# Performance work log

Hardware: AMD Instinct MI355X
Metric: run time of the kernel (lower is better)

The kernel has to match this reference:

```python
import jax, jax.numpy as jnp
import numpy as np

HEADS = 8
DIM_HEAD = 64
SCALE = DIM_HEAD ** -0.5


def setup_inputs() -> dict:
    key = jax.random.key(0)
    ks = jax.random.split(key, 6)
    B, S, D = 4, 2048, 512
    return {
        "hidden_states": jax.random.normal(ks[0], (B, S, D), jnp.float32),
        "Wq": jax.random.normal(ks[1], (D, D), jnp.float32) * (D ** -0.5),
        "Wk": jax.random.normal(ks[2], (D, D), jnp.float32) * (D ** -0.5),
        "Wv": jax.random.normal(ks[3], (D, D), jnp.float32) * (D ** -0.5),
        "Wo": jax.random.normal(ks[4], (D, D), jnp.float32) * (D ** -0.5),
        "bo": jnp.zeros((D,), jnp.float32),
    }


def reference(hidden_states, Wq, Wk, Wv, Wo, bo):
    B, S, D = hidden_states.shape
    H, Dh = HEADS, DIM_HEAD
    # Linear projections (torch Linear: x @ W.T; weights here stored as [D, D] used directly)
    q = hidden_states @ Wq  # [B,S,D]
    k = hidden_states @ Wk
    v = hidden_states @ Wv
    # head_to_batch_dim: [B,S,D] -> [B,H,S,Dh]
    q = q.reshape(B, S, H, Dh).transpose(0, 2, 1, 3)
    k = k.reshape(B, S, H, Dh).transpose(0, 2, 1, 3)
    v = v.reshape(B, S, H, Dh).transpose(0, 2, 1, 3)
    # scaled dot-product attention, scores materialized as in baddbmm path
    scores = jnp.einsum("bhqd,bhkd->bhqk", q, k) * SCALE  # [B,H,S,S]
    probs = jax.nn.softmax(scores, axis=-1)
    out = jnp.einsum("bhqk,bhkd->bhqd", probs, v)  # [B,H,S,Dh]
    # batch_to_head_dim: [B,H,S,Dh] -> [B,S,D]
    out = out.transpose(0, 2, 1, 3).reshape(B, S, D)
    # output projection (Dropout with p=0 is identity)
    return out @ Wo + bo
```

## Files before the change

kernel.cpp:

```cpp
#include <hip/hip_runtime.h>
#include <cstdint>
#include <cstddef>


typedef __bf16 bf16;
typedef __bf16 bf16x4_t __attribute__((ext_vector_type(4)));
typedef __bf16 bf16x8_t __attribute__((ext_vector_type(8)));
typedef float  floatx4  __attribute__((ext_vector_type(4)));
typedef short  shortx4  __attribute__((ext_vector_type(4)));
typedef uint32_t u32x4  __attribute__((ext_vector_type(4)));

#define NB   4
#define SEQ  2048
#define DM   512
#define NH   8
#define DH   64
#define MTOT (NB * SEQ)


__device__ __forceinline__ void gload16(const void* g, void* l) {
    __builtin_amdgcn_global_load_lds((const __attribute__((address_space(1))) unsigned int*)g,
                                     (__attribute__((address_space(3))) unsigned int*)l,
                                     16, 0, 0);
}

__device__ __forceinline__ shortx4 pack4(floatx4 v) {
    union { bf16x4_t h; shortx4 s; } u;
    u.h = (bf16x4_t){ (bf16)v[0], (bf16)v[1], (bf16)v[2], (bf16)v[3] };
    return u.s;
}

__global__ __launch_bounds__(256) void cvt_x(const float* __restrict__ x, bf16* __restrict__ xb) {
    int i = (blockIdx.x * 256 + threadIdx.x) * 4;
    float4 v = *(const float4*)(x + i);
    bf16x4_t o = { (bf16)v.x, (bf16)v.y, (bf16)v.z, (bf16)v.w };
    *(bf16x4_t*)(xb + i) = o;
}

__global__ __launch_bounds__(256) void prep_w(const float* __restrict__ Wq, const float* __restrict__ Wk,
                                              const float* __restrict__ Wv, const float* __restrict__ Wo,
                                              bf16* __restrict__ Wqkvt, bf16* __restrict__ Wot) {
    __shared__ float T[64][65];
    const int tid = threadIdx.x;
    const int m = blockIdx.z;
    const int k0 = blockIdx.x * 64, n0 = blockIdx.y * 64;
    const float* W = (m == 0) ? Wq : (m == 1) ? Wk : (m == 2) ? Wv : Wo;
    const float scale = (m == 0) ? 0.18033688011112042f : 1.0f;
#pragma unroll
    for (int p = 0; p < 4; p++) {
        int row = p * 16 + (tid >> 4), col = (tid & 15) * 4;
        float4 v = *(const float4*)(W + (size_t)(k0 + row) * DM + n0 + col);
        T[row][col + 0] = v.x * scale; T[row][col + 1] = v.y * scale;
        T[row][col + 2] = v.z * scale; T[row][col + 3] = v.w * scale;
    }
    __syncthreads();
#pragma unroll
    for (int p = 0; p < 4; p++) {
        int nr = p * 16 + (tid >> 4), kc = (tid & 15) * 4;
        bf16x4_t o = { (bf16)T[kc][nr], (bf16)T[kc + 1][nr], (bf16)T[kc + 2][nr], (bf16)T[kc + 3][nr] };
        bf16* dst = (m < 3) ? (Wqkvt + ((size_t)(m * DM + n0 + nr)) * DM + k0 + kc)
                            : (Wot + (size_t)(n0 + nr) * DM + k0 + kc);
        *(bf16x4_t*)dst = o;
    }
}

__global__ __launch_bounds__(256) void gemm_qkv(
        const bf16* __restrict__ A, const bf16* __restrict__ Bt,
        bf16* __restrict__ Qh, bf16* __restrict__ Kh, bf16* __restrict__ Vt) {
    __shared__ __attribute__((aligned(16))) bf16 Sm[2][128 * 64];
    bf16* As = Sm[0]; bf16* Bs = Sm[1];
    const int tid = threadIdx.x;
    const int wave = tid >> 6, lane = tid & 63;
    const int l15 = lane & 15, quad = lane >> 4, h7 = l15 & 7;
    const int m0 = blockIdx.x * 128, n0 = blockIdx.y * 128;
    const int mw = (wave >> 1) * 64, nw = (wave & 1) * 64;
    const int srow = lane >> 3, sc = (lane & 7) ^ srow;

    floatx4 zero = {0.f, 0.f, 0.f, 0.f};
    floatx4 acc[4][4];
#pragma unroll
    for (int i = 0; i < 4; i++)
#pragma unroll
        for (int j = 0; j < 4; j++) acc[i][j] = zero;

    for (int k0 = 0; k0 < DM; k0 += 64) {
#pragma unroll
        for (int t = 0; t < 4; t++) {
            int row = wave * 32 + t * 8 + srow;
            gload16(A  + (size_t)(m0 + row) * DM + k0 + sc * 8, As + (wave * 32 + t * 8) * 64);
            gload16(Bt + (size_t)(n0 + row) * DM + k0 + sc * 8, Bs + (wave * 32 + t * 8) * 64);
        }
        __syncthreads();
#pragma unroll
        for (int ks = 0; ks < 2; ks++) {
            bf16x8_t af[4], bfr[4];
#pragma unroll
            for (int i = 0; i < 4; i++)
                af[i] = *(const bf16x8_t*)(As + (mw + i * 16 + l15) * 64 + (((ks * 4 + quad) ^ h7) * 8));
#pragma unroll
            for (int j = 0; j < 4; j++)
                bfr[j] = *(const bf16x8_t*)(Bs + (nw + j * 16 + l15) * 64 + (((ks * 4 + quad) ^ h7) * 8));
#pragma unroll
            for (int i = 0; i < 4; i++)
#pragma unroll
                for (int j = 0; j < 4; j++)
                    acc[i][j] = __builtin_amdgcn_mfma_f32_16x16x32_bf16(af[i], bfr[j], acc[i][j], 0, 0, 0);
        }
        __syncthreads();
    }

    bf16* E = (bf16*)Sm;
    const int sect = n0 >> 9;
    const int bq = m0 >> 11;
    if (sect < 3 && (n0 >> 9) != 2) {}
    if (sect != 2) {
        bf16* dstbase = (sect == 0) ? Qh : Kh;
#pragma unroll
        for (int p = 0; p < 2; p++) {
            if ((wave >> 1) == p) {
#pragma unroll
                for (int i = 0; i < 4; i++)
#pragma unroll
                    for (int j = 0; j < 4; j++)
#pragma unroll
                        for (int r = 0; r < 4; r++)
                            E[(i * 16 + quad * 4 + r) * 136 + nw + j * 16 + l15] = (bf16)acc[i][j][r];
            }
            __syncthreads();
#pragma unroll
            for (int pp = 0; pp < 4; pp++) {
                int idx = pp * 256 + tid;
                int rowl = idx >> 4, chunk = idx & 15;
                u32x4 v = *(const u32x4*)(E + rowl * 136 + chunk * 8);
                int mm = m0 + p * 64 + rowl;
                int s = mm & (SEQ - 1);
                int n = n0 + chunk * 8;
                int h = (n >> 6) & 7, d = n & 63;
                *(u32x4*)(dstbase + (((size_t)(bq * NH + h)) * SEQ + s) * DH + d) = v;
            }
            __syncthreads();
        }
    } else {
#pragma unroll
        for (int p = 0; p < 2; p++) {
            if ((wave & 1) == p) {
#pragma unroll
                for (int i = 0; i < 4; i++)
#pragma unroll
                    for (int j = 0; j < 4; j++)
                        *(shortx4*)(E + (j * 16 + l15) * 136 + mw + i * 16 + quad * 4) = pack4(acc[i][j]);
            }
            __syncthreads();
#pragma unroll
            for (int pp = 0; pp < 4; pp++) {
                int idx = pp * 256 + tid;
                int rowl = idx >> 4, chunk = idx & 15;
                u32x4 v = *(const u32x4*)(E + rowl * 136 + chunk * 8);
                int n = n0 + p * 64 + rowl;
                int h = (n >> 6) & 7, d = n & 63;
                int s = (m0 & (SEQ - 1)) + chunk * 8;
                *(u32x4*)(Vt + (((size_t)(bq * NH + h)) * DH + d) * SEQ + s) = v;
            }
            __syncthreads();
        }
    }
}

__global__ __launch_bounds__(256) void gemm_out(
        const bf16* __restrict__ A, const bf16* __restrict__ Bt,
        const float* __restrict__ bo, float* __restrict__ out) {
    __shared__ __attribute__((aligned(16))) bf16 As[64 * 64];
    __shared__ __attribute__((aligned(16))) bf16 Bs[128 * 64];
    const int tid = threadIdx.x;
    const int wave = tid >> 6, lane = tid & 63;
    const int l15 = lane & 15, quad = lane >> 4, h7 = l15 & 7;
    const int m0 = blockIdx.x * 64, n0 = blockIdx.y * 128;
    const int nw = wave * 32;
    const int srow = lane >> 3, sc = (lane & 7) ^ srow;

    floatx4 zero = {0.f, 0.f, 0.f, 0.f};
    floatx4 acc[4][2];
#pragma unroll
    for (int i = 0; i < 4; i++)
#pragma unroll
        for (int j = 0; j < 2; j++) acc[i][j] = zero;

    for (int k0 = 0; k0 < DM; k0 += 64) {
#pragma unroll
        for (int t = 0; t < 2; t++) {
            int row = wave * 16 + t * 8 + srow;
            gload16(A + (size_t)(m0 + row) * DM + k0 + sc * 8, As + (wave * 16 + t * 8) * 64);
        }
#pragma unroll
        for (int t = 0; t < 4; t++) {
            int row = wave * 32 + t * 8 + srow;
            gload16(Bt + (size_t)(n0 + row) * DM + k0 + sc * 8, Bs + (wave * 32 + t * 8) * 64);
        }
        __syncthreads();
#pragma unroll
        for (int ks = 0; ks < 2; ks++) {
            bf16x8_t af[4], bfr[2];
#pragma unroll
            for (int i = 0; i < 4; i++)
                af[i] = *(const bf16x8_t*)(As + (i * 16 + l15) * 64 + (((ks * 4 + quad) ^ h7) * 8));
#pragma unroll
            for (int j = 0; j < 2; j++)
                bfr[j] = *(const bf16x8_t*)(Bs + (nw + j * 16 + l15) * 64 + (((ks * 4 + quad) ^ h7) * 8));
#pragma unroll
            for (int i = 0; i < 4; i++)
#pragma unroll
                for (int j = 0; j < 2; j++)
                    acc[i][j] = __builtin_amdgcn_mfma_f32_16x16x32_bf16(af[i], bfr[j], acc[i][j], 0, 0, 0);
        }
        __syncthreads();
    }
#pragma unroll
    for (int i = 0; i < 4; i++)
#pragma unroll
        for (int j = 0; j < 2; j++)
#pragma unroll
            for (int r = 0; r < 4; r++) {
                int m = m0 + i * 16 + quad * 4 + r;
                int n = n0 + nw + j * 16 + l15;
                out[(size_t)m * DM + n] = acc[i][j][r] + bo[n];
            }
}

__global__ __launch_bounds__(256, 2) void flash_attn(
        const bf16* __restrict__ Q, const bf16* __restrict__ Kh,
        const bf16* __restrict__ Vt, bf16* __restrict__ Ob) {
    __shared__ __attribute__((aligned(16))) bf16 SMEM[4 * 8192];
    const int tid = threadIdx.x;
    const int wave = tid >> 6, lane = tid & 63;
    const int l15 = lane & 15, quad = lane >> 4, h7 = l15 & 7;
    const int qh = wave >> 1, kvh = wave & 1;
    const int qt = blockIdx.x & 15, bh = blockIdx.x >> 4;
    const int q0 = qt * 128;
    const bf16* Kb = Kh + (size_t)bh * SEQ * DH;
    const bf16* Vb = Vt + (size_t)bh * DH * SEQ;

    bf16x8_t aq[4][2];
#pragma unroll
    for (int sub = 0; sub < 4; sub++) {
        const bf16* qr = Q + ((size_t)bh * SEQ + q0 + qh * 64 + sub * 16 + l15) * DH;
        aq[sub][0] = *(const bf16x8_t*)(qr + quad * 8);
        aq[sub][1] = *(const bf16x8_t*)(qr + 32 + quad * 8);
    }

    const int srow = lane >> 3, sc = (lane & 7) ^ srow;
    auto stage = [&](int buf, int kv0) {
#pragma unroll
        for (int t = 0; t < 2; t++) {
            int rb = wave * 16 + t * 8;
            gload16(Kb + (size_t)(kv0 + rb + srow) * DH + sc * 8, SMEM + buf * 8192 + rb * 64);
            gload16(Vb + (size_t)(rb + srow) * SEQ + kv0 + sc * 8, SMEM + buf * 8192 + 4096 + rb * 64);
        }
    };

    floatx4 zero = {0.f, 0.f, 0.f, 0.f};
    floatx4 oacc[4][4];
    float l_run[4] = {0.f, 0.f, 0.f, 0.f};
#pragma unroll
    for (int sub = 0; sub < 4; sub++)
#pragma unroll
        for (int d = 0; d < 4; d++) oacc[sub][d] = zero;

    stage(0, 0);
    stage(1, 64);
    for (int seg = 0; seg < 16; seg++) {
        __syncthreads();
        if (seg < 15) {
            stage((2 * seg + 2) & 3, (2 * seg + 2) * 64);
            stage((2 * seg + 3) & 3, (2 * seg + 3) * 64);
        }
#pragma unroll
        for (int half = 0; half < 2; half++) {
            const bf16* Ks = SMEM + ((2 * seg + half) & 3) * 8192;
            const bf16* Vs = Ks + 4096;
            floatx4 st[4][2];
#pragma unroll
            for (int nsl = 0; nsl < 2; nsl++) {
                int row = (kvh * 2 + nsl) * 16 + l15;
                const bf16* kr = Ks + row * 64;
                bf16x8_t k0 = *(const bf16x8_t*)(kr + ((quad ^ h7) * 8));
                bf16x8_t k1 = *(const bf16x8_t*)(kr + (((4 + quad) ^ h7) * 8));
#pragma unroll
                for (int sub = 0; sub < 4; sub++) {
                    floatx4 a = zero;
                    a = __builtin_amdgcn_mfma_f32_16x16x32_bf16(k0, aq[sub][0], a, 0, 0, 0);
                    a = __builtin_amdgcn_mfma_f32_16x16x32_bf16(k1, aq[sub][1], a, 0, 0, 0);
                    st[sub][nsl] = a;
                }
            }
#pragma unroll
            for (int sub = 0; sub < 4; sub++) {
                float s = 0.f;
#pragma unroll
                for (int nsl = 0; nsl < 2; nsl++)
#pragma unroll
                    for (int r = 0; r < 4; r++) {
                        float p = __builtin_amdgcn_exp2f(st[sub][nsl][r]);
                        st[sub][nsl][r] = p;
                        s += p;
                    }
                l_run[sub] += s;
            }
#pragma unroll
            for (int cl = 0; cl < 2; cl++) {
                int c = kvh * 2 + cl;
                shortx4 ap[4];
#pragma unroll
                for (int sub = 0; sub < 4; sub++) ap[sub] = pack4(st[sub][cl]);
                int cc = 2 * c + (quad >> 1);
#pragma unroll
                for (int d = 0; d < 4; d++) {
                    const bf16* vr = Vs + (d * 16 + l15) * 64;
                    shortx4 bv = *(const shortx4*)(vr + ((cc ^ h7) * 8) + (quad & 1) * 4);
#pragma unroll
                    for (int sub = 0; sub < 4; sub++)
                        oacc[sub][d] = __builtin_amdgcn_mfma_f32_16x16x16bf16_1k(ap[sub], bv, oacc[sub][d], 0, 0, 0);
                }
            }
        }
    }

    float lf[4];
#pragma unroll
    for (int sub = 0; sub < 4; sub++) {
        float l = l_run[sub];
        l += __shfl_xor(l, 16, 64);
        l += __shfl_xor(l, 32, 64);
        lf[sub] = l;
    }
    __syncthreads();
    float* blob = (float*)SMEM + qh * (68 * 64);
    if (kvh == 1) {
#pragma unroll
        for (int sub = 0; sub < 4; sub++)
#pragma unroll
            for (int d = 0; d < 4; d++)
#pragma unroll
                for (int r = 0; r < 4; r++)
                    blob[((sub * 4 + d) * 4 + r) * 64 + lane] = oacc[sub][d][r];
#pragma unroll
        for (int sub = 0; sub < 4; sub++)
            blob[(64 + sub) * 64 + lane] = lf[sub];
    }
    __syncthreads();
    if (kvh == 0) {
#pragma unroll
        for (int sub = 0; sub < 4; sub++)
#pragma unroll
            for (int d = 0; d < 4; d++)
#pragma unroll
                for (int r = 0; r < 4; r++)
                    oacc[sub][d][r] += blob[((sub * 4 + d) * 4 + r) * 64 + lane];
#pragma unroll
        for (int sub = 0; sub < 4; sub++)
            lf[sub] += blob[(64 + sub) * 64 + lane];

        const int b = bh >> 3, h = bh & 7;
#pragma unroll
        for (int sub = 0; sub < 4; sub++) {
            float linv[4];
#pragma unroll
            for (int r = 0; r < 4; r++) linv[r] = 1.0f / __shfl(lf[sub], quad * 4 + r, 64);
#pragma unroll
            for (int d = 0; d < 4; d++)
#pragma unroll
                for (int r = 0; r < 4; r++) {
                    int s = q0 + qh * 64 + sub * 16 + quad * 4 + r;
                    Ob[((size_t)b * SEQ + s) * DM + h * DH + d * 16 + l15] = (bf16)(oacc[sub][d][r] * linv[r]);
                }
        }
    }
}

extern "C" void kernel_launch(void* const* d_in, const int* in_sizes, int n_in,
                              void* d_out, int out_size, void* d_ws, size_t ws_size,
                              hipStream_t stream) {
    const float* X  = (const float*)d_in[0];
    const float* Wq = (const float*)d_in[1];
    const float* Wk = (const float*)d_in[2];
    const float* Wv = (const float*)d_in[3];
    const float* Wo = (const float*)d_in[4];
    const float* bo = (const float*)d_in[5];
    float* out = (float*)d_out;

    char* ws = (char*)d_ws;
    bf16* Xb    = (bf16*)(ws + 0);
    bf16* Wqkvt = (bf16*)(ws + 8388608);
    bf16* Wot   = (bf16*)(ws + 9961472);
    bf16* Qh    = (bf16*)(ws + 10485760);
    bf16* Kh    = (bf16*)(ws + 18874368);
    bf16* Vt    = (bf16*)(ws + 27262976);
    bf16* Ob    = (bf16*)(ws + 35651584);

    cvt_x<<<MTOT * DM / 1024, 256, 0, stream>>>(X, Xb);
    prep_w<<<dim3(8, 8, 4), 256, 0, stream>>>(Wq, Wk, Wv, Wo, Wqkvt, Wot);
    gemm_qkv<<<dim3(MTOT / 128, 1536 / 128), 256, 0, stream>>>(Xb, Wqkvt, Qh, Kh, Vt);
    flash_attn<<<NB * NH * (SEQ / 128), 256, 0, stream>>>(Qh, Kh, Vt, Ob);
    gemm_out<<<dim3(MTOT / 64, DM / 128), 256, 0, stream>>>(Ob, Wot, bo, out);
}
```

Baseline: 160.7 us.

## Halve attention LDS to raise occupancy, merge prep kernels into one launch

Flash attention now double-buffers single 64-row KV tiles instead of quad-buffering pairs, which halves shared memory. Its launch bound rises from 2 to 4 blocks per SM. The final cross-wave reduction is split into two phases so it fits in the smaller LDS buffer. The X-conversion and weight-prep kernels are merged into one launch to cut launch overhead. The risks are register spills under the tighter launch bound and less prefetch depth to hide memory latency.

```diff
diff --git a/kernel.cpp b/kernel.cpp
--- a/kernel.cpp
+++ b/kernel.cpp
@@ -30,20 +30,23 @@
     return u.s;
 }
 
-__global__ __launch_bounds__(256) void cvt_x(const float* __restrict__ x, bf16* __restrict__ xb) {
-    int i = (blockIdx.x * 256 + threadIdx.x) * 4;
-    float4 v = *(const float4*)(x + i);
-    bf16x4_t o = { (bf16)v.x, (bf16)v.y, (bf16)v.z, (bf16)v.w };
-    *(bf16x4_t*)(xb + i) = o;
-}
-
-__global__ __launch_bounds__(256) void prep_w(const float* __restrict__ Wq, const float* __restrict__ Wk,
-                                              const float* __restrict__ Wv, const float* __restrict__ Wo,
-                                              bf16* __restrict__ Wqkvt, bf16* __restrict__ Wot) {
+__global__ __launch_bounds__(256) void prep(
+        const float* __restrict__ X, const float* __restrict__ Wq, const float* __restrict__ Wk,
+        const float* __restrict__ Wv, const float* __restrict__ Wo,
+        bf16* __restrict__ xb, bf16* __restrict__ Wqkvt, bf16* __restrict__ Wot) {
     __shared__ float T[64][65];
     const int tid = threadIdx.x;
-    const int m = blockIdx.z;
-    const int k0 = blockIdx.x * 64, n0 = blockIdx.y * 64;
+    const int bx = blockIdx.x;
+    if (bx < 4096) {
+        int i = (bx * 256 + tid) * 4;
+        float4 v = *(const float4*)(X + i);
+        bf16x4_t o = { (bf16)v.x, (bf16)v.y, (bf16)v.z, (bf16)v.w };
+        *(bf16x4_t*)(xb + i) = o;
+        return;
+    }
+    const int idx = bx - 4096;
+    const int m = idx >> 6;
+    const int k0 = ((idx >> 3) & 7) * 64, n0 = (idx & 7) * 64;
     const float* W = (m == 0) ? Wq : (m == 1) ? Wk : (m == 2) ? Wv : Wo;
     const float scale = (m == 0) ? 0.18033688011112042f : 1.0f;
 #pragma unroll
@@ -112,7 +115,6 @@
     bf16* E = (bf16*)Sm;
     const int sect = n0 >> 9;
     const int bq = m0 >> 11;
-    if (sect < 3 && (n0 >> 9) != 2) {}
     if (sect != 2) {
         bf16* dstbase = (sect == 0) ? Qh : Kh;
 #pragma unroll
@@ -226,10 +228,10 @@
             }
 }
 
-__global__ __launch_bounds__(256, 2) void flash_attn(
+__global__ __launch_bounds__(256, 4) void flash_attn(
         const bf16* __restrict__ Q, const bf16* __restrict__ Kh,
         const bf16* __restrict__ Vt, bf16* __restrict__ Ob) {
-    __shared__ __attribute__((aligned(16))) bf16 SMEM[4 * 8192];
+    __shared__ __attribute__((aligned(16))) bf16 SMEM[2 * 8192];
     const int tid = threadIdx.x;
     const int wave = tid >> 6, lane = tid & 63;
     const int l15 = lane & 15, quad = lane >> 4, h7 = l15 & 7;
@@ -266,60 +268,54 @@
         for (int d = 0; d < 4; d++) oacc[sub][d] = zero;
 
     stage(0, 0);
-    stage(1, 64);
-    for (int seg = 0; seg < 16; seg++) {
-        __syncthreads();
-        if (seg < 15) {
-            stage((2 * seg + 2) & 3, (2 * seg + 2) * 64);
-            stage((2 * seg + 3) & 3, (2 * seg + 3) * 64);
-        }
-#pragma unroll
-        for (int half = 0; half < 2; half++) {
-            const bf16* Ks = SMEM + ((2 * seg + half) & 3) * 8192;
-            const bf16* Vs = Ks + 4096;
-            floatx4 st[4][2];
-#pragma unroll
-            for (int nsl = 0; nsl < 2; nsl++) {
-                int row = (kvh * 2 + nsl) * 16 + l15;
-                const bf16* kr = Ks + row * 64;
-                bf16x8_t k0 = *(const bf16x8_t*)(kr + ((quad ^ h7) * 8));
-                bf16x8_t k1 = *(const bf16x8_t*)(kr + (((4 + quad) ^ h7) * 8));
-#pragma unroll
-                for (int sub = 0; sub < 4; sub++) {
-                    floatx4 a = zero;
-                    a = __builtin_amdgcn_mfma_f32_16x16x32_bf16(k0, aq[sub][0], a, 0, 0, 0);
-                    a = __builtin_amdgcn_mfma_f32_16x16x32_bf16(k1, aq[sub][1], a, 0, 0, 0);
-                    st[sub][nsl] = a;
+    for (int it = 0; it < SEQ / 64; it++) {
+        __syncthreads();
+        if (it + 1 < SEQ / 64) stage((it + 1) & 1, (it + 1) * 64);
+        const bf16* Ks = SMEM + (it & 1) * 8192;
+        const bf16* Vs = Ks + 4096;
+
+        floatx4 st[4][2];
+#pragma unroll
+        for (int nsl = 0; nsl < 2; nsl++) {
+            int row = (kvh * 2 + nsl) * 16 + l15;
+            const bf16* kr = Ks + row * 64;
+            bf16x8_t k0 = *(const bf16x8_t*)(kr + ((quad ^ h7) * 8));
+            bf16x8_t k1 = *(const bf16x8_t*)(kr + (((4 + quad) ^ h7) * 8));
+#pragma unroll
+            for (int sub = 0; sub < 4; sub++) {
+                floatx4 a = zero;
+                a = __builtin_amdgcn_mfma_f32_16x16x32_bf16(k0, aq[sub][0], a, 0, 0, 0);
+                a = __builtin_amdgcn_mfma_f32_16x16x32_bf16(k1, aq[sub][1], a, 0, 0, 0);
+                st[sub][nsl] = a;
+            }
+        }
+#pragma unroll
+        for (int sub = 0; sub < 4; sub++) {
+            float s = 0.f;
+#pragma unroll
+            for (int nsl = 0; nsl < 2; nsl++)
+#pragma unroll
+                for (int r = 0; r < 4; r++) {
+                    float p = __builtin_amdgcn_exp2f(st[sub][nsl][r]);
+                    st[sub][nsl][r] = p;
+                    s += p;
                 }
-            }
-#pragma unroll
-            for (int sub = 0; sub < 4; sub++) {
-                float s = 0.f;
-#pragma unroll
-                for (int nsl = 0; nsl < 2; nsl++)
-#pragma unroll
-                    for (int r = 0; r < 4; r++) {
-                        float p = __builtin_amdgcn_exp2f(st[sub][nsl][r]);
-                        st[sub][nsl][r] = p;
-                        s += p;
-                    }
-                l_run[sub] += s;
-            }
-#pragma unroll
-            for (int cl = 0; cl < 2; cl++) {
-                int c = kvh * 2 + cl;
-                shortx4 ap[4];
-#pragma unroll
-                for (int sub = 0; sub < 4; sub++) ap[sub] = pack4(st[sub][cl]);
-                int cc = 2 * c + (quad >> 1);
-#pragma unroll
-                for (int d = 0; d < 4; d++) {
-                    const bf16* vr = Vs + (d * 16 + l15) * 64;
-                    shortx4 bv = *(const shortx4*)(vr + ((cc ^ h7) * 8) + (quad & 1) * 4);
-#pragma unroll
-                    for (int sub = 0; sub < 4; sub++)
-                        oacc[sub][d] = __builtin_amdgcn_mfma_f32_16x16x16bf16_1k(ap[sub], bv, oacc[sub][d], 0, 0, 0);
-                }
+            l_run[sub] += s;
+        }
+#pragma unroll
+        for (int cl = 0; cl < 2; cl++) {
+            int c = kvh * 2 + cl;
+            shortx4 ap[4];
+#pragma unroll
+            for (int sub = 0; sub < 4; sub++) ap[sub] = pack4(st[sub][cl]);
+            int cc = 2 * c + (quad >> 1);
+#pragma unroll
+            for (int d = 0; d < 4; d++) {
+                const bf16* vr = Vs + (d * 16 + l15) * 64;
+                shortx4 bv = *(const shortx4*)(vr + ((cc ^ h7) * 8) + (quad & 1) * 4);
+#pragma unroll
+                for (int sub = 0; sub < 4; sub++)
+                    oacc[sub][d] = __builtin_amdgcn_mfma_f32_16x16x16bf16_1k(ap[sub], bv, oacc[sub][d], 0, 0, 0);
             }
         }
     }
@@ -332,47 +328,43 @@
         l += __shfl_xor(l, 32, 64);
         lf[sub] = l;
     }
+    const int b = bh >> 3, h = bh & 7;
+    float* blob = (float*)SMEM;
     __syncthreads();
-    float* blob = (float*)SMEM + qh * (68 * 64);
-    if (kvh == 1) {
-#pragma unroll
-        for (int sub = 0; sub < 4; sub++)
-#pragma unroll
-            for (int d = 0; d < 4; d++)
-#pragma unroll
-                for (int r = 0; r < 4; r++)
-                    blob[((sub * 4 + d) * 4 + r) * 64 + lane] = oacc[sub][d][r];
-#pragma unroll
-        for (int sub = 0; sub < 4; sub++)
-            blob[(64 + sub) * 64 + lane] = lf[sub];
-    }
-    __syncthreads();
-    if (kvh == 0) {
-#pragma unroll
-        for (int sub = 0; sub < 4; sub++)
-#pragma unroll
-            for (int d = 0; d < 4; d++)
-#pragma unroll
-                for (int r = 0; r < 4; r++)
-                    oacc[sub][d][r] += blob[((sub * 4 + d) * 4 + r) * 64 + lane];
-#pragma unroll
-        for (int sub = 0; sub < 4; sub++)
-            lf[sub] += blob[(64 + sub) * 64 + lane];
-
-        const int b = bh >> 3, h = bh & 7;
-#pragma unroll
-        for (int sub = 0; sub < 4; sub++) {
-            float linv[4];
-#pragma unroll
-            for (int r = 0; r < 4; r++) linv[r] = 1.0f / __shfl(lf[sub], quad * 4 + r, 64);
-#pragma unroll
-            for (int d = 0; d < 4; d++)
-#pragma unroll
-                for (int r = 0; r < 4; r++) {
-                    int s = q0 + qh * 64 + sub * 16 + quad * 4 + r;
-                    Ob[((size_t)b * SEQ + s) * DM + h * DH + d * 16 + l15] = (bf16)(oacc[sub][d][r] * linv[r]);
-                }
-        }
+#pragma unroll
+    for (int ph = 0; ph < 2; ph++) {
+        if (kvh == 1) {
+#pragma unroll
+            for (int sl = 0; sl < 2; sl++) {
+                int sub = ph * 2 + sl;
+#pragma unroll
+                for (int d = 0; d < 4; d++)
+#pragma unroll
+                    for (int r = 0; r < 4; r++)
+                        blob[qh * 2176 + ((sl * 4 + d) * 4 + r) * 64 + lane] = oacc[sub][d][r];
+                blob[qh * 2176 + (32 + sl) * 64 + lane] = lf[sub];
+            }
+        }
+        __syncthreads();
+        if (kvh == 0) {
+#pragma unroll
+            for (int sl = 0; sl < 2; sl++) {
+                int sub = ph * 2 + sl;
+                float lt = lf[sub] + blob[qh * 2176 + (32 + sl) * 64 + lane];
+                float linv[4];
+#pragma unroll
+                for (int r = 0; r < 4; r++) linv[r] = 1.0f / __shfl(lt, quad * 4 + r, 64);
+#pragma unroll
+                for (int d = 0; d < 4; d++)
+#pragma unroll
+                    for (int r = 0; r < 4; r++) {
+                        float o = oacc[sub][d][r] + blob[qh * 2176 + ((sl * 4 + d) * 4 + r) * 64 + lane];
+                        int s = q0 + qh * 64 + sub * 16 + quad * 4 + r;
+                        Ob[((size_t)b * SEQ + s) * DM + h * DH + d * 16 + l15] = (bf16)(o * linv[r]);
+                    }
+            }
+        }
+        __syncthreads();
     }
 }
 
@@ -396,8 +388,7 @@
     bf16* Vt    = (bf16*)(ws + 27262976);
     bf16* Ob    = (bf16*)(ws + 35651584);
 
-    cvt_x<<<MTOT * DM / 1024, 256, 0, stream>>>(X, Xb);
-    prep_w<<<dim3(8, 8, 4), 256, 0, stream>>>(Wq, Wk, Wv, Wo, Wqkvt, Wot);
+    prep<<<4096 + 256, 256, 0, stream>>>(X, Wq, Wk, Wv, Wo, Xb, Wqkvt, Wot);
     gemm_qkv<<<dim3(MTOT / 128, 1536 / 128), 256, 0, stream>>>(Xb, Wqkvt, Qh, Kh, Vt);
     flash_attn<<<NB * NH * (SEQ / 128), 256, 0, stream>>>(Qh, Kh, Vt, Ob);
     gemm_out<<<dim3(MTOT / 64, DM / 128), 256, 0, stream>>>(Ob, Wot, bo, out);
```

Result: slower. 284.6 us (+77.1%).
